# Optimization experiments

Measured on AMD Instinct MI355X. Metric: run time of the kernel, lower is better.

Reference implementation:

```python
import jax, jax.numpy as jnp
import numpy as np

EPS = 1e-12  # matches F.normalize default eps


def _l2norm(a, axis):
    n = jnp.sqrt(jnp.sum(a * a, axis=axis, keepdims=True))
    return a / jnp.maximum(n, EPS)


def setup_inputs() -> dict:
    key = jax.random.key(0)
    k1, k2, k3, k4, k5 = jax.random.split(key, 5)
    B, H, W = 512, 64, 64
    Y, Z = 32768, 1000
    x = jax.random.normal(k1, (B, H, W), dtype=jnp.float32)
    z = jax.random.randint(k2, (B,), 0, Z, dtype=jnp.int64 if jax.config.jax_enable_x64 else jnp.int32).astype(jnp.int32)
    x2y_w = jax.random.uniform(k3, (Y, H * W), dtype=jnp.float32)
    y2z_w = jax.random.uniform(k4, (Z, Y), dtype=jnp.float32)
    y_age = jax.random.randint(k5, (1, Y), 0, 3, dtype=jnp.int32)
    return {"x": x, "z": z, "x2y_w": x2y_w, "y2z_w": y2z_w, "y_age": y_age, "per_item": 1}


def reference(x, z, x2y_w, y2z_w, y_age, per_item):
    # DN.forward, mode='test'
    B = x.shape[0]
    Y = x2y_w.shape[0]
    xf = _l2norm(x.reshape(B, -1), axis=1)              # [B, X]
    w_xy = _l2norm(x2y_w, axis=1)                       # row-normalized [Y, X]
    w_yz = _l2norm(y2z_w, axis=1)                       # row-normalized [Z, Y]
    y_bu = jnp.einsum('bx,yx->by', xf, w_xy)            # bottom-up response [B, Y]
    active = (y_age >= 1).astype(y_bu.dtype)            # [1, Y] age gate
    y_pre = y_bu * active                               # gated responses
    # top_k_competition(flag=0): top-1 winner-take-all -> one-hot response
    winner = jnp.argmax(y_pre, axis=1)                  # [B]
    y_resp = jax.nn.one_hot(winner, Y, dtype=y_pre.dtype)  # [B, Y]
    out = jnp.einsum('by,zy->bz', y_resp, w_yz)         # [B, Z]
    return out
```

## Files before the change

### kernel.cpp

```cpp
#include <hip/hip_runtime.h>
#include <math.h>


typedef _Float16 half8 __attribute__((ext_vector_type(8)));
typedef __attribute__((ext_vector_type(16))) float f32x16;
typedef unsigned long long ull;

#define TAU 0.006f
#define CAP 1572864u
#define LCAP 1536u

__device__ __forceinline__ unsigned pk2h(float a, float b) {
    union { _Float16 h; unsigned short u; } ca, cb;
    ca.h = (_Float16)a; cb.h = (_Float16)b;
    return (unsigned)ca.u | ((unsigned)cb.u << 16);
}

__device__ __forceinline__ ull packkey(float v, unsigned y) {
    unsigned m = __float_as_uint(v);
    m = (v >= 0.f) ? (m | 0x80000000u) : ~m;
    return ((ull)m << 32) | (ull)(0x7FFFFFFFu - y);
}

__global__ __launch_bounds__(512) void init_ctrl(const int* __restrict__ age,
                                                 ull* __restrict__ win,
                                                 unsigned* __restrict__ cnt) {
    const int t = threadIdx.x;
    int fi = 0x7fffffff;
    for (int y = t; y < 32768; y += 512)
        if (age[y] < 1) fi = min(fi, y);
    __shared__ int red[512];
    red[t] = fi;
    __syncthreads();
    for (int s = 256; s; s >>= 1) {
        if (t < s) red[t] = min(red[t], red[t + s]);
        __syncthreads();
    }
    const int f = red[0];
    const ull seed = (f < 32768) ? packkey(0.0f, (unsigned)f) : packkey(-1e30f, 0u);
    win[t] = seed;
    if (t == 0) *cnt = 0u;
}

__global__ __launch_bounds__(512) void convert_x(const float* __restrict__ x,
                                                 uint4* __restrict__ xf16) {
    const int o = blockIdx.x * 512 + threadIdx.x;
    const int lane = o & 63;
    const int ks = (o >> 6) & 1;
    const int mi = (o >> 7) & 1;
    const int wm = (o >> 8) & 7;
    const int t  = o >> 11;
    const int row = (wm << 6) + (mi << 5) + (lane & 31);
    const int col = (t << 5) + (ks << 4) + ((lane >> 5) << 3);
    const float* src = x + (size_t)row * 4096 + col;
    const float4 a = *(const float4*)src;
    const float4 b = *(const float4*)(src + 4);
    uint4 u;
    u.x = pk2h(a.x, a.y); u.y = pk2h(a.z, a.w);
    u.z = pk2h(b.x, b.y); u.w = pk2h(b.z, b.w);
    xf16[o] = u;
}

__global__ __launch_bounds__(256) void row_norms(const float* __restrict__ src,
                                                 float* __restrict__ dst, int cols) {
    const int r = blockIdx.x;
    const float* row = src + (size_t)r * cols;
    const int t = threadIdx.x;
    float s = 0.f;
    const int nIter = cols >> 10;
    for (int i = 0; i < nIter; ++i) {
        const float4 v = *reinterpret_cast<const float4*>(row + (((i << 8) + t) << 2));
        s = fmaf(v.x, v.x, s); s = fmaf(v.y, v.y, s);
        s = fmaf(v.z, v.z, s); s = fmaf(v.w, v.w, s);
    }
    #pragma unroll
    for (int off = 32; off; off >>= 1) s += __shfl_down(s, off);
    __shared__ float red[4];
    if ((t & 63) == 0) red[t >> 6] = s;
    __syncthreads();
    if (t == 0) dst[r] = sqrtf(red[0] + red[1] + red[2] + red[3]);
}

__global__ __launch_bounds__(512, 2) void gemm_f16(
    const float* __restrict__ w,
    const uint4* __restrict__ xf16,
    const int*  __restrict__ age,
    float* __restrict__ cand,
    float2* __restrict__ ent,
    unsigned* __restrict__ cnt)
{
    __shared__ uint4 Bl[2][512];
    __shared__ float ny_inv[128];
    __shared__ float rowmaxs[512];
    __shared__ float2 lent[LCAP];
    __shared__ unsigned lcnt, gbase;

    const int tid = threadIdx.x;
    const int y0 = blockIdx.x << 7;

    const int rB = tid >> 2, q = tid & 3;
    const int wiB = (rB << 2) + (q ^ (rB & 3));
    const float* bP = w + (size_t)(y0 + rB) * 4096 + (q << 3);

    const int lane = tid & 63, wm = tid >> 6;
    const int kh = lane >> 5, cc = lane & 3;
    const uint4* aP = xf16 + (wm << 8) + lane;

    const int rb0 = ((lane & 31)      ) << 2;
    const int rb1 = ((lane & 31) +  32) << 2;
    const int rb2 = ((lane & 31) +  64) << 2;
    const int rb3 = ((lane & 31) +  96) << 2;
    const int s0 = kh ^ cc, s1 = (2 | kh) ^ cc;

    f32x16 am0n0 = (f32x16)0.f, am0n1 = (f32x16)0.f;
    f32x16 am0n2 = (f32x16)0.f, am0n3 = (f32x16)0.f;
    f32x16 am1n0 = (f32x16)0.f, am1n1 = (f32x16)0.f;
    f32x16 am1n2 = (f32x16)0.f, am1n3 = (f32x16)0.f;

    half8 pa00, pa01, pa10, pa11;
    half8 qa00, qa01, qa10, qa11;
    half8 g00, g10, g20, g30;
    half8 g01, g11, g21, g31;
    float4 SAa, SAb;
    float4 SBa, SBb;
    float nyacc = 0.f;

#define MF(a, b, c) __builtin_amdgcn_mfma_f32_32x32x16_f16(a, b, c, 0, 0, 0)
#define LG0 asm volatile("s_waitcnt lgkmcnt(0)" ::: "memory")
#define SBR __builtin_amdgcn_sched_barrier(0)

#define LOADA(S, tt) { const uint4* p_ = aP + ((size_t)(tt) << 11); \
    S##00 = *(const half8*)(p_);        S##01 = *(const half8*)(p_ + 64); \
    S##10 = *(const half8*)(p_ + 128);  S##11 = *(const half8*)(p_ + 192); }

#define LOADW(S, tt) { const float* p_ = bP + ((tt) << 5); \
    S##a = *(const float4*)p_; S##b = *(const float4*)(p_ + 4); }

#define STOREB(buf, S) { uint4 u_; \
    u_.x = pk2h(S##a.x, S##a.y); u_.y = pk2h(S##a.z, S##a.w); \
    u_.z = pk2h(S##b.x, S##b.y); u_.w = pk2h(S##b.z, S##b.w); \
    Bl[buf][wiB] = u_; \
    nyacc = fmaf(S##a.x, S##a.x, nyacc); nyacc = fmaf(S##a.y, S##a.y, nyacc); \
    nyacc = fmaf(S##a.z, S##a.z, nyacc); nyacc = fmaf(S##a.w, S##a.w, nyacc); \
    nyacc = fmaf(S##b.x, S##b.x, nyacc); nyacc = fmaf(S##b.y, S##b.y, nyacc); \
    nyacc = fmaf(S##b.z, S##b.z, nyacc); nyacc = fmaf(S##b.w, S##b.w, nyacc); }

#define LDB(cur) { \
    g00 = *(const half8*)&Bl[cur][rb0 + s0]; g01 = *(const half8*)&Bl[cur][rb0 + s1]; \
    g10 = *(const half8*)&Bl[cur][rb1 + s0]; g11 = *(const half8*)&Bl[cur][rb1 + s1]; \
    g20 = *(const half8*)&Bl[cur][rb2 + s0]; g21 = *(const half8*)&Bl[cur][rb2 + s1]; \
    g30 = *(const half8*)&Bl[cur][rb3 + s0]; g31 = *(const half8*)&Bl[cur][rb3 + s1]; }

#define MFMA16(S) { \
    am0n0 = MF(S##00, g00, am0n0); am0n1 = MF(S##00, g10, am0n1); \
    am0n2 = MF(S##00, g20, am0n2); am0n3 = MF(S##00, g30, am0n3); \
    am1n0 = MF(S##10, g00, am1n0); am1n1 = MF(S##10, g10, am1n1); \
    am1n2 = MF(S##10, g20, am1n2); am1n3 = MF(S##10, g30, am1n3); \
    am0n0 = MF(S##01, g01, am0n0); am0n1 = MF(S##01, g11, am0n1); \
    am0n2 = MF(S##01, g21, am0n2); am0n3 = MF(S##01, g31, am0n3); \
    am1n0 = MF(S##11, g01, am1n0); am1n1 = MF(S##11, g11, am1n1); \
    am1n2 = MF(S##11, g21, am1n2); am1n3 = MF(S##11, g31, am1n3); }

#define TILE(cur, tt, AC, AN, WS, GA, GW) { \
    LDB(cur); \
    if (GA) LOADA(AN, (tt) + 1); \
    if (GA) STOREB((cur) ^ 1, WS); \
    if (GW) LOADW(WS, (tt) + 3); \
    MFMA16(AC); \
    LG0; SBR; \
    __builtin_amdgcn_s_barrier(); }

    LOADW(SA, 0);
    LOADA(pa, 0);
    STOREB(0, SA);
    LOADW(SA, 1);
    LOADW(SB, 2);
    LG0; SBR;
    __builtin_amdgcn_s_barrier();

    for (int t = 0; t < 124; t += 2) {
        TILE(0, t,     pa, qa, SA, 1, 1)
        TILE(1, t + 1, qa, pa, SB, 1, 1)
    }
    TILE(0, 124, pa, qa, SA, 1, 1)
    TILE(1, 125, qa, pa, SB, 1, 0)
    TILE(0, 126, pa, qa, SA, 1, 0)
    TILE(1, 127, qa, pa, SB, 0, 0)

    float s_ = nyacc;
    s_ += __shfl_xor(s_, 1);
    s_ += __shfl_xor(s_, 2);
    if (q == 0) ny_inv[rB] = 1.0f / fmaxf(sqrtf(s_), 1e-12f);
    if (tid == 0) lcnt = 0u;
    __syncthreads();

    const int yl0 = (lane & 31), yl1 = yl0 + 32, yl2 = yl0 + 64, yl3 = yl0 + 96;
    const float scl0 = ny_inv[yl0], scl1 = ny_inv[yl1];
    const float scl2 = ny_inv[yl2], scl3 = ny_inv[yl3];
    const int act0 = age[y0 + yl0] >= 1, act1 = age[y0 + yl1] >= 1;
    const int act2 = age[y0 + yl2] >= 1, act3 = age[y0 + yl3] >= 1;
    const int yb0 = y0 + yl0, yb1 = y0 + yl1, yb2 = y0 + yl2, yb3 = y0 + yl3;
    const int rbase = (wm << 6) + (kh << 2);

#define ROWMAX(A0, A1, A2, A3, mi5) \
    _Pragma("unroll") for (int v = 0; v < 16; ++v) { \
        float bv = fmaxf( \
            fmaxf(act0 ? A0[v] * scl0 : 0.f, act1 ? A1[v] * scl1 : 0.f), \
            fmaxf(act2 ? A2[v] * scl2 : 0.f, act3 ? A3[v] * scl3 : 0.f)); \
        _Pragma("unroll") for (int off = 1; off < 32; off <<= 1) \
            bv = fmaxf(bv, __shfl_xor(bv, off)); \
        if ((lane & 31) == 0) \
            rowmaxs[rbase + (mi5) + (v & 3) + ((v >> 2) << 3)] = bv; \
    }
    ROWMAX(am0n0, am0n1, am0n2, am0n3, 0)
    ROWMAX(am1n0, am1n1, am1n2, am1n3, 32)
    __syncthreads();
    cand[(size_t)tid * 256 + blockIdx.x] = rowmaxs[tid];
    __syncthreads();

#define APP1(ACv, actk, sclk, ybk, r_) { \
    if (actk) { const float sc_ = (ACv) * sclk; \
        if (sc_ >= rowmaxs[r_] - TAU) { \
            const unsigned ix_ = atomicAdd(&lcnt, 1u); \
            if (ix_ < LCAP) lent[ix_] = make_float2(sc_, \
                __uint_as_float(((unsigned)(r_) << 16) | (unsigned)(ybk))); } } }

#define APPEND(A0, A1, A2, A3, mi5) \
    _Pragma("unroll") for (int v = 0; v < 16; ++v) { \
        const int r_ = rbase + (mi5) + (v & 3) + ((v >> 2) << 3); \
        APP1(A0[v], act0, scl0, yb0, r_) \
        APP1(A1[v], act1, scl1, yb1, r_) \
        APP1(A2[v], act2, scl2, yb2, r_) \
        APP1(A3[v], act3, scl3, yb3, r_) }
    APPEND(am0n0, am0n1, am0n2, am0n3, 0)
    APPEND(am1n0, am1n1, am1n2, am1n3, 32)
    __syncthreads();
    if (tid == 0) gbase = atomicAdd(cnt, min(lcnt, LCAP));
    __syncthreads();
    const unsigned nL = min(lcnt, LCAP);
    for (unsigned i = tid; i < nL; i += 512) {
        const unsigned gi = gbase + i;
        if (gi < CAP) ent[gi] = lent[i];
    }
#undef MF
#undef LG0
#undef SBR
#undef LOADA
#undef LOADW
#undef STOREB
#undef LDB
#undef MFMA16
#undef TILE
#undef ROWMAX
#undef APP1
#undef APPEND
}

__global__ __launch_bounds__(256) void reduce_gmax(const float* __restrict__ cand,
                                                   float* __restrict__ gmax) {
    const int b = blockIdx.x, t = threadIdx.x;
    float m = cand[(size_t)b * 256 + t];
    #pragma unroll
    for (int off = 32; off; off >>= 1) m = fmaxf(m, __shfl_xor(m, off));
    __shared__ float sm[4];
    if ((t & 63) == 0) sm[t >> 6] = m;
    __syncthreads();
    if (t == 0) gmax[b] = fmaxf(fmaxf(sm[0], sm[1]), fmaxf(sm[2], sm[3]));
}

__global__ __launch_bounds__(256) void rescore(
    const float* __restrict__ x, const float* __restrict__ w,
    const float* __restrict__ gmax, const float2* __restrict__ ent,
    const unsigned* __restrict__ cnt, ull* __restrict__ win)
{
    const unsigned n = min(*cnt, CAP);
    const int lane = threadIdx.x & 63;
    const unsigned wid = (blockIdx.x * 256 + threadIdx.x) >> 6;
    const unsigned nwv = (gridDim.x * 256) >> 6;
    for (unsigned base = wid << 6; base < n; base += (nwv << 6)) {
        const unsigned e = base + (unsigned)lane;
        unsigned by = 0u;
        bool ok = false;
        if (e < n) {
            const float2 en = ent[e];
            by = __float_as_uint(en.y);
            ok = en.x >= gmax[by >> 16] - TAU;
        }
        ull m = __ballot(ok);
        while (m) {
            const int s = __ffsll((ull)m) - 1;
            m &= m - 1;
            const unsigned bys = __shfl(by, s);
            const unsigned b = bys >> 16, y = bys & 0xffffu;
            const float4* xr = (const float4*)(x + (size_t)b * 4096);
            const float4* wr = (const float4*)(w + (size_t)y * 4096);
            float sdot = 0.f, nn = 0.f;
            #pragma unroll
            for (int k = 0; k < 16; ++k) {
                const float4 xv = xr[(k << 6) + lane];
                const float4 wv = wr[(k << 6) + lane];
                sdot = fmaf(xv.x, wv.x, sdot); sdot = fmaf(xv.y, wv.y, sdot);
                sdot = fmaf(xv.z, wv.z, sdot); sdot = fmaf(xv.w, wv.w, sdot);
                nn = fmaf(wv.x, wv.x, nn); nn = fmaf(wv.y, wv.y, nn);
                nn = fmaf(wv.z, wv.z, nn); nn = fmaf(wv.w, wv.w, nn);
            }
            #pragma unroll
            for (int off = 32; off; off >>= 1) {
                sdot += __shfl_xor(sdot, off);
                nn   += __shfl_xor(nn, off);
            }
            if (lane == 0) {
                const float sc = sdot / fmaxf(sqrtf(nn), 1e-12f);
                atomicMax(win + b, packkey(sc, y));
            }
        }
    }
}

__global__ __launch_bounds__(256) void gather_out(const float* __restrict__ y2z,
                                                  const float* __restrict__ nz,
                                                  const ull* __restrict__ win,
                                                  float* __restrict__ out) {
    const int g = blockIdx.x * 256 + threadIdx.x;
    if (g >= 512 * 1000) return;
    const int b = g / 1000, z = g - b * 1000;
    const unsigned lo = (unsigned)(win[b] & 0xffffffffull);
    const int yw = (int)(0x7FFFFFFFu - lo);
    out[g] = y2z[(size_t)z * 32768 + yw] / fmaxf(nz[z], 1e-12f);
}

extern "C" void kernel_launch(void* const* d_in, const int* in_sizes, int n_in,
                              void* d_out, int out_size, void* d_ws, size_t ws_size,
                              hipStream_t stream) {
    const float* x     = (const float*)d_in[0];
    const float* x2y_w = (const float*)d_in[2];
    const float* y2z_w = (const float*)d_in[3];
    const int*   y_age = (const int*)d_in[4];
    float* out = (float*)d_out;

    char* p = (char*)d_ws;
    float*    cand = (float*)p;
    float*    nz   = (float*)(p + 524288);
    float*    gmax = (float*)(p + 528384);
    ull*      win  = (ull*)(p + 530432);
    unsigned* cnt  = (unsigned*)(p + 534528);
    uint4*    xf16 = (uint4*)(p + 534592);
    float2*   ent  = (float2*)(p + 4728896);

    init_ctrl<<<1, 512, 0, stream>>>(y_age, win, cnt);
    convert_x<<<512, 512, 0, stream>>>(x, xf16);
    row_norms<<<1000, 256, 0, stream>>>(y2z_w, nz, 32768);

    gemm_f16<<<256, 512, 0, stream>>>(x2y_w, xf16, y_age, cand, ent, cnt);
    reduce_gmax<<<512, 256, 0, stream>>>(cand, gmax);
    rescore<<<256, 256, 0, stream>>>(x, x2y_w, gmax, ent, cnt, win);
    gather_out<<<(512 * 1000 + 255) / 256, 256, 0, stream>>>(y2z_w, nz, win, out);
}
```

Measured before the change: 298.2 us.

## Deepen LDS ring to four buffers and barrier every other tile

Expands the shared-memory B staging from double to quad buffering, with four register sets of prefetched weight rows loaded six tiles ahead. The goal is to hide global-load latency better and to halve the number of workgroup barriers, since writes now land two buffers ahead of reads. This costs more LDS and registers, which may hurt occupancy at two blocks per CU. The loop also now evaluates bounds conditions inside the unrolled body.

After: 311.1 us. +4.3%, slower.

```diff
diff --git a/kernel.cpp b/kernel.cpp
--- a/kernel.cpp
+++ b/kernel.cpp
@@ -89,7 +89,7 @@
     float2* __restrict__ ent,
     unsigned* __restrict__ cnt)
 {
-    __shared__ uint4 Bl[2][512];
+    __shared__ uint4 Bl[4][512];
     __shared__ float ny_inv[128];
     __shared__ float rowmaxs[512];
     __shared__ float2 lent[LCAP];
@@ -121,8 +121,8 @@
     half8 qa00, qa01, qa10, qa11;
     half8 g00, g10, g20, g30;
     half8 g01, g11, g21, g31;
-    float4 SAa, SAb;
-    float4 SBa, SBb;
+    float4 SAa, SAb, SBa, SBb;
+    float4 SCa, SCb, SDa, SDb;
     float nyacc = 0.f;
 
 #define MF(a, b, c) __builtin_amdgcn_mfma_f32_32x32x16_f16(a, b, c, 0, 0, 0)
@@ -161,31 +161,28 @@
     am1n0 = MF(S##11, g01, am1n0); am1n1 = MF(S##11, g11, am1n1); \
     am1n2 = MF(S##11, g21, am1n2); am1n3 = MF(S##11, g31, am1n3); }
 
-#define TILE(cur, tt, AC, AN, WS, GA, GW) { \
-    LDB(cur); \
-    if (GA) LOADA(AN, (tt) + 1); \
-    if (GA) STOREB((cur) ^ 1, WS); \
-    if (GW) LOADW(WS, (tt) + 3); \
+#define TILE(bR, bW, tt, AC, AN, WS, DOBAR) { \
+    LDB(bR); \
+    if ((tt) + 1 < 128) LOADA(AN, (tt) + 1); \
+    if ((tt) + 2 < 128) STOREB(bW, WS); \
+    if ((tt) + 6 < 128) LOADW(WS, (tt) + 6); \
     MFMA16(AC); \
-    LG0; SBR; \
-    __builtin_amdgcn_s_barrier(); }
-
-    LOADW(SA, 0);
+    if (DOBAR) { LG0; SBR; __builtin_amdgcn_s_barrier(); } }
+
+    LOADW(SA, 0); LOADW(SB, 1);
     LOADA(pa, 0);
     STOREB(0, SA);
-    LOADW(SA, 1);
-    LOADW(SB, 2);
+    STOREB(1, SB);
+    LOADW(SA, 2); LOADW(SB, 3); LOADW(SC, 4); LOADW(SD, 5);
     LG0; SBR;
     __builtin_amdgcn_s_barrier();
 
-    for (int t = 0; t < 124; t += 2) {
-        TILE(0, t,     pa, qa, SA, 1, 1)
-        TILE(1, t + 1, qa, pa, SB, 1, 1)
-    }
-    TILE(0, 124, pa, qa, SA, 1, 1)
-    TILE(1, 125, qa, pa, SB, 1, 0)
-    TILE(0, 126, pa, qa, SA, 1, 0)
-    TILE(1, 127, qa, pa, SB, 0, 0)
+    for (int t = 0; t < 128; t += 4) {
+        TILE(0, 2, t,     pa, qa, SA, 0)
+        TILE(1, 3, t + 1, qa, pa, SB, 1)
+        TILE(2, 0, t + 2, pa, qa, SC, 0)
+        TILE(3, 1, t + 3, qa, pa, SD, 1)
+    }
 
     float s_ = nyacc;
     s_ += __shfl_xor(s_, 1);
```
